# Optimization experiments

Hardware: AMD Instinct MI355X
Metric: run time of the kernel (lower is better)

## Reference

```python
import jax, jax.numpy as jnp
import numpy as np

B, T, D = 1, 2048, 1024
H = 16
SEM_DIM, GEO_DIM, ATTN_DIM = 512, 512, 1024
ROPE_BASE = 10000.0
NEG = -1e9


def setup_inputs() -> dict:
    key = jax.random.key(0)
    ks = jax.random.split(key, 10)
    s = 0.02
    return {
        "x": jax.random.normal(ks[0], (B, T, D), jnp.float32),
        "wq_sem": jax.random.normal(ks[1], (D, SEM_DIM), jnp.float32) * s,
        "wk_sem": jax.random.normal(ks[2], (D, SEM_DIM), jnp.float32) * s,
        "wq_geo": jax.random.normal(ks[3], (D, GEO_DIM), jnp.float32) * s,
        "wk_geo": jax.random.normal(ks[4], (D, GEO_DIM), jnp.float32) * s,
        "wv": jax.random.normal(ks[5], (D, ATTN_DIM), jnp.float32) * s,
        "wo": jax.random.normal(ks[6], (ATTN_DIM, D), jnp.float32) * s,
        "k_sem_null": jax.random.normal(ks[7], (SEM_DIM,), jnp.float32) * s,
        "k_geo_null": jax.random.normal(ks[8], (GEO_DIM,), jnp.float32) * s,
        "v_null": jax.random.normal(ks[9], (ATTN_DIM,), jnp.float32) * s,
    }


def _heads(y, hd):
    b, t, _ = y.shape
    return y.reshape(b, t, H, hd).transpose(0, 2, 1, 3)  # [B,H,T,hd]


def _rope(x, cos, sin):
    # x: [B,H,T,hd], cos/sin: [T,hd//2] (rotate-half convention)
    hd = x.shape[-1]
    x1, x2 = x[..., : hd // 2], x[..., hd // 2 :]
    c = cos[None, None]
    sn = sin[None, None]
    return jnp.concatenate([x1 * c - x2 * sn, x2 * c + x1 * sn], axis=-1)


def _forward(x, wq_sem, wk_sem, wq_geo, wk_geo, wv, wo, k_sem_null, k_geo_null, v_null):
    b, t, _ = x.shape
    sem_hd = wq_sem.shape[1] // H
    geo_hd = wq_geo.shape[1] // H
    v_hd = wv.shape[1] // H
    sem_scale = 1.0 / np.sqrt(sem_hd)
    geo_scale = 1.0 / np.sqrt(geo_hd)

    qs = _heads(x @ wq_sem, sem_hd)
    ks = _heads(x @ wk_sem, sem_hd)
    qg = _heads(x @ wq_geo, geo_hd)
    kg = _heads(x @ wk_geo, geo_hd)
    v = _heads(x @ wv, v_hd)

    # RoPE on geometric branch only
    pos = jnp.arange(t, dtype=jnp.float32)
    inv_freq = 1.0 / (ROPE_BASE ** (jnp.arange(0, geo_hd, 2, dtype=jnp.float32) / geo_hd))
    ang = pos[:, None] * inv_freq[None, :]  # [T, geo_hd//2]
    cos, sin = jnp.cos(ang), jnp.sin(ang)
    qg = _rope(qg, cos, sin)
    kg = _rope(kg, cos, sin)

    # prepend null KV slot (not rotated, always attendable)
    ksn = jnp.broadcast_to(k_sem_null.reshape(1, 1, H, sem_hd).transpose(0, 2, 1, 3), (b, H, 1, sem_hd))
    kgn = jnp.broadcast_to(k_geo_null.reshape(1, 1, H, geo_hd).transpose(0, 2, 1, 3), (b, H, 1, geo_hd))
    vn = jnp.broadcast_to(v_null.reshape(1, 1, H, v_hd).transpose(0, 2, 1, 3), (b, H, 1, v_hd))
    ks_full = jnp.concatenate([ksn, ks], axis=2)  # [B,H,T+1,sem_hd]
    kg_full = jnp.concatenate([kgn, kg], axis=2)
    v_full = jnp.concatenate([vn, v], axis=2)

    # decoupled scores in fp32: sem*sem_scale + geo*geo_scale
    scores = (
        jnp.einsum("bhqd,bhkd->bhqk", qs, ks_full).astype(jnp.float32) * sem_scale
        + jnp.einsum("bhqd,bhkd->bhqk", qg, kg_full).astype(jnp.float32) * geo_scale
    )

    # causal mask over real tokens; null slot (key index 0) always visible
    causal = jnp.tril(jnp.ones((t, t), dtype=bool))
    mask = jnp.concatenate([jnp.ones((t, 1), dtype=bool), causal], axis=1)  # [T, T+1]
    scores = jnp.where(mask[None, None], scores, NEG)

    probs = jax.nn.softmax(scores, axis=-1).astype(v.dtype)
    out = jnp.einsum("bhqk,bhkd->bhqd", probs, v_full)  # [B,H,T,v_hd]
    out = out.transpose(0, 2, 1, 3).reshape(b, t, H * v_hd)
    return out @ wo


def reference(x, wq_sem, wk_sem, wq_geo, wk_geo, wv, wo, k_sem_null, k_geo_null, v_null):
    return _forward(x, wq_sem, wk_sem, wq_geo, wk_geo, wv, wo, k_sem_null, k_geo_null, v_null)
```

## Files before the change

### kernel.cpp

```cpp
#include <hip/hip_runtime.h>
#include <hip/hip_bf16.h>

typedef __hip_bfloat16 bf16;
typedef __attribute__((ext_vector_type(8))) short bf16x8;
typedef __attribute__((ext_vector_type(4))) short bf16x4;
typedef __attribute__((ext_vector_type(4))) float f32x4;

#define TSEQ   2048
#define DMODEL 1024
#define NHEAD  16
#define KST    2112
#define SCALE  0.17677669529663687f
#define LN1E4_16 0.5756462732485115f

__device__ __forceinline__ unsigned short f2bf(float f) {
    union { bf16 h; unsigned short u; } x;
    x.h = __float2bfloat16(f);
    return x.u;
}
__device__ __forceinline__ float bf2f(unsigned short u) {
    return __uint_as_float(((unsigned int)u) << 16);
}

__device__ __forceinline__ void gload_lds16(const void* g, void* l) {
    __builtin_amdgcn_global_load_lds(
        (const __attribute__((address_space(1))) void*)g,
        (__attribute__((address_space(3))) void*)l, 16, 0, 0);
}

__global__ __launch_bounds__(256) void prep_all(
    const float* __restrict__ X,
    const float* __restrict__ wqs, const float* __restrict__ wks,
    const float* __restrict__ wqg, const float* __restrict__ wkg,
    const float* __restrict__ wv,  const float* __restrict__ wo,
    const float* __restrict__ ksn, const float* __restrict__ kgn,
    const float* __restrict__ vn,
    unsigned short* __restrict__ Xb,
    unsigned short* __restrict__ WcatT, unsigned short* __restrict__ WoT,
    unsigned short* __restrict__ Kc, unsigned short* __restrict__ Vg)
{
    __shared__ float T[64][65];
    const int bx = blockIdx.x;
    const int tid = threadIdx.x;
    if (bx < 2048) {
        int i = (bx * 256 + tid) * 4;
        float4 v = *(const float4*)(X + i);
        ushort4 o;
        o.x = f2bf(v.x); o.y = f2bf(v.y); o.z = f2bf(v.z); o.w = f2bf(v.w);
        *(ushort4*)(Xb + i) = o;
    } else if (bx < 3584) {
        const int idx = bx - 2048;
        const int z = idx >> 8, rem = idx & 255;
        const int cx = rem & 15, ry = rem >> 4;
        const float* src; unsigned short* dst; int C;
        switch (z) {
            case 0: src = wqs; dst = WcatT;               C = 512;  break;
            case 1: src = wks; dst = WcatT + 512  * 1024; C = 512;  break;
            case 2: src = wqg; dst = WcatT + 1024 * 1024; C = 512;  break;
            case 3: src = wkg; dst = WcatT + 1536 * 1024; C = 512;  break;
            case 4: src = wv;  dst = WcatT + 2048 * 1024; C = 1024; break;
            default: src = wo; dst = WoT;                 C = 1024; break;
        }
        const int c0 = cx * 64;
        if (c0 >= C) return;
        const int r0 = ry * 64;
        #pragma unroll
        for (int i = 0; i < 16; ++i) {
            int id2 = tid + 256 * i;
            int r = id2 >> 6, c = id2 & 63;
            T[r][c] = src[(size_t)(r0 + r) * C + c0 + c];
        }
        __syncthreads();
        #pragma unroll
        for (int i = 0; i < 16; ++i) {
            int id2 = tid + 256 * i;
            int cc = id2 >> 6, rr = id2 & 63;
            dst[(size_t)(c0 + cc) * 1024 + r0 + rr] = f2bf(T[rr][cc]);
        }
    } else {
        const int h = bx - 3584;
        const int d = tid & 63, g = tid >> 6;
        if (g == 0)
            Kc[((size_t)h * KST + 0) * 64 + d] =
                f2bf(d < 32 ? ksn[h * 32 + d] : kgn[h * 32 + d - 32]);
        if (g == 1)
            Vg[((size_t)h * 64 + d) * KST + 0] = f2bf(vn[h * 64 + d]);
        for (int fk = 2049 + g; fk < KST; fk += 4) {
            Kc[((size_t)h * KST + fk) * 64 + d] = 0;
            Vg[((size_t)h * 64 + d) * KST + fk] = 0;
        }
    }
}

__global__ __launch_bounds__(256) void gemm_proj_fused(
    const unsigned short* __restrict__ A,
    const unsigned short* __restrict__ Bt,
    unsigned short* __restrict__ Qc,
    unsigned short* __restrict__ Kc,
    unsigned short* __restrict__ Vg)
{
    __shared__ __align__(16) unsigned short Abuf[64 * 64];
    __shared__ __align__(16) unsigned short Bbuf[128 * 64];
    const int n0 = blockIdx.x * 128, m0 = blockIdx.y * 64;
    const int tid = threadIdx.x, l = tid & 63, wv = tid >> 6;
    const int wr = wv >> 1, wc = wv & 1;
    const int lr = l & 15, lg = l >> 4;

    f32x4 acc[2][4];
    #pragma unroll
    for (int i = 0; i < 2; ++i)
        #pragma unroll
        for (int j = 0; j < 4; ++j) acc[i][j] = (f32x4){0.f, 0.f, 0.f, 0.f};

    for (int k0 = 0; k0 < 1024; k0 += 64) {
        #pragma unroll
        for (int i = 0; i < 2; ++i) {
            int c = wv * 128 + i * 64 + l;
            int row = c >> 3, sseg = (c & 7) ^ (row & 7);
            gload_lds16(A + (size_t)(m0 + row) * 1024 + k0 + sseg * 8,
                        &Abuf[(wv * 128 + i * 64) * 8]);
        }
        #pragma unroll
        for (int i = 0; i < 4; ++i) {
            int c = wv * 256 + i * 64 + l;
            int row = c >> 3, sseg = (c & 7) ^ (row & 7);
            gload_lds16(Bt + (size_t)(n0 + row) * 1024 + k0 + sseg * 8,
                        &Bbuf[(wv * 256 + i * 64) * 8]);
        }
        __syncthreads();
        #pragma unroll
        for (int ks = 0; ks < 2; ++ks) {
            bf16x8 af[2], bfv[4];
            #pragma unroll
            for (int mf = 0; mf < 2; ++mf) {
                int rr = wr * 32 + mf * 16 + lr;
                int seg = (ks * 4 + lg) ^ (rr & 7);
                af[mf] = *(const bf16x8*)&Abuf[rr * 64 + seg * 8];
            }
            #pragma unroll
            for (int nf = 0; nf < 4; ++nf) {
                int rr = wc * 64 + nf * 16 + lr;
                int seg = (ks * 4 + lg) ^ (rr & 7);
                bfv[nf] = *(const bf16x8*)&Bbuf[rr * 64 + seg * 8];
            }
            #pragma unroll
            for (int mf = 0; mf < 2; ++mf)
                #pragma unroll
                for (int nf = 0; nf < 4; ++nf)
                    acc[mf][nf] = __builtin_amdgcn_mfma_f32_16x16x32_bf16(
                        af[mf], bfv[nf], acc[mf][nf], 0, 0, 0);
        }
        __syncthreads();
    }

    const int sec = n0 >> 9;
    if (sec <= 1) {
        unsigned short* dst = (sec == 0) ? Qc : Kc;
        const int tstr  = (sec == 0) ? TSEQ : KST;
        const int fkoff = (sec == 0) ? 0 : 1;
        const float sc  = (sec == 0) ? SCALE : 1.0f;
        #pragma unroll
        for (int mf = 0; mf < 2; ++mf)
            #pragma unroll
            for (int nf = 0; nf < 4; ++nf) {
                int col = (n0 & 511) + wc * 64 + nf * 16 + lr;
                int h = col >> 5, d = col & 31;
                #pragma unroll
                for (int reg = 0; reg < 4; ++reg) {
                    int q = m0 + wr * 32 + mf * 16 + lg * 4 + reg;
                    dst[((size_t)h * tstr + q + fkoff) * 64 + d] =
                        f2bf(acc[mf][nf][reg] * sc);
                }
            }
    } else if (sec <= 3) {
        unsigned short* dst = (sec == 2) ? Qc : Kc;
        const int tstr  = (sec == 2) ? TSEQ : KST;
        const int fkoff = (sec == 2) ? 0 : 1;
        const float sc  = (sec == 2) ? SCALE : 1.0f;
        const float invf = __expf(-(float)lr * LN1E4_16);
        #pragma unroll
        for (int mf = 0; mf < 2; ++mf)
            #pragma unroll
            for (int reg = 0; reg < 4; ++reg) {
                int q = m0 + wr * 32 + mf * 16 + lg * 4 + reg;
                float s, c;
                __sincosf((float)q * invf, &s, &c);
                #pragma unroll
                for (int nfp = 0; nfp < 2; ++nfp) {
                    int nf0 = nfp * 2;
                    int colbase = (n0 & 511) + wc * 64 + nf0 * 16;
                    int h = colbase >> 5;
                    float x1 = acc[mf][nf0][reg], x2 = acc[mf][nf0 + 1][reg];
                    size_t base = ((size_t)h * tstr + q + fkoff) * 64 + 32;
                    dst[base + lr]      = f2bf((x1 * c - x2 * s) * sc);
                    dst[base + lr + 16] = f2bf((x2 * c + x1 * s) * sc);
                }
            }
    } else {
        #pragma unroll
        for (int nf = 0; nf < 4; ++nf) {
            int colr = (n0 - 2048) + wc * 64 + nf * 16 + lr;
            int h = colr >> 6, dv = colr & 63;
            size_t rowbase = ((size_t)h * 64 + dv) * KST;
            #pragma unroll
            for (int mf = 0; mf < 2; ++mf)
                #pragma unroll
                for (int reg = 0; reg < 4; ++reg) {
                    int q = m0 + wr * 32 + mf * 16 + lg * 4 + reg;
                    Vg[rowbase + q + 1] = f2bf(acc[mf][nf][reg]);
                }
        }
    }
}

__global__ __launch_bounds__(256) void gemm_out(const unsigned short* __restrict__ A,
                                                const unsigned short* __restrict__ Bt,
                                                float* __restrict__ C)
{
    __shared__ __align__(16) unsigned short Abuf[64 * 64];
    __shared__ __align__(16) unsigned short Bbuf[128 * 64];
    const int n0 = blockIdx.x * 128, m0 = blockIdx.y * 64;
    const int tid = threadIdx.x, l = tid & 63, wv = tid >> 6;
    const int wr = wv >> 1, wc = wv & 1;
    const int lr = l & 15, lg = l >> 4;

    f32x4 acc[2][4];
    #pragma unroll
    for (int i = 0; i < 2; ++i)
        #pragma unroll
        for (int j = 0; j < 4; ++j) acc[i][j] = (f32x4){0.f, 0.f, 0.f, 0.f};

    for (int k0 = 0; k0 < 1024; k0 += 64) {
        #pragma unroll
        for (int i = 0; i < 2; ++i) {
            int c = wv * 128 + i * 64 + l;
            int row = c >> 3, sseg = (c & 7) ^ (row & 7);
            gload_lds16(A + (size_t)(m0 + row) * 1024 + k0 + sseg * 8,
                        &Abuf[(wv * 128 + i * 64) * 8]);
        }
        #pragma unroll
        for (int i = 0; i < 4; ++i) {
            int c = wv * 256 + i * 64 + l;
            int row = c >> 3, sseg = (c & 7) ^ (row & 7);
            gload_lds16(Bt + (size_t)(n0 + row) * 1024 + k0 + sseg * 8,
                        &Bbuf[(wv * 256 + i * 64) * 8]);
        }
        __syncthreads();
        #pragma unroll
        for (int ks = 0; ks < 2; ++ks) {
            bf16x8 af[2], bfv[4];
            #pragma unroll
            for (int mf = 0; mf < 2; ++mf) {
                int rr = wr * 32 + mf * 16 + lr;
                int seg = (ks * 4 + lg) ^ (rr & 7);
                af[mf] = *(const bf16x8*)&Abuf[rr * 64 + seg * 8];
            }
            #pragma unroll
            for (int nf = 0; nf < 4; ++nf) {
                int rr = wc * 64 + nf * 16 + lr;
                int seg = (ks * 4 + lg) ^ (rr & 7);
                bfv[nf] = *(const bf16x8*)&Bbuf[rr * 64 + seg * 8];
            }
            #pragma unroll
            for (int mf = 0; mf < 2; ++mf)
                #pragma unroll
                for (int nf = 0; nf < 4; ++nf)
                    acc[mf][nf] = __builtin_amdgcn_mfma_f32_16x16x32_bf16(
                        af[mf], bfv[nf], acc[mf][nf], 0, 0, 0);
        }
        __syncthreads();
    }
    #pragma unroll
    for (int mf = 0; mf < 2; ++mf)
        #pragma unroll
        for (int nf = 0; nf < 4; ++nf)
            #pragma unroll
            for (int reg = 0; reg < 4; ++reg) {
                int row = m0 + wr * 32 + mf * 16 + lg * 4 + reg;
                int col = n0 + wc * 64 + nf * 16 + lr;
                C[(size_t)row * DMODEL + col] = acc[mf][nf][reg];
            }
}

__global__ __launch_bounds__(256) void attn_mfma(
    const unsigned short* __restrict__ Qc,
    const unsigned short* __restrict__ Kc,
    const unsigned short* __restrict__ Vg,
    unsigned short* __restrict__ attnO,
    unsigned short* __restrict__ OpA,
    unsigned short* __restrict__ OpB,
    float2* __restrict__ ml)
{
    __shared__ __align__(16) unsigned short KsL[2][64 * 64];
    __shared__ __align__(16) unsigned short VsL[2][64 * 64];
    __shared__ __align__(16) unsigned short Ps[128 * 64];

    const int ib = blockIdx.x;
    const int hp = ib & 7;
    const int j  = ib >> 3;
    const int h  = hp * 2 + (j & 1);
    const int item = j >> 1;

    int qb, part, np;
    {
        int i = item;
        if (i < 16)      { np = 4; qb = 15 - (i >> 2); part = i & 3; }
        else if (i < 28) { int jj = i - 16; np = 3; qb = 11 - jj / 3; part = jj % 3; }
        else if (i < 38) { int jj = i - 28; np = 2; qb = 7 - (jj >> 1); part = jj & 1; }
        else             { np = 1; qb = 2 - (i - 38); part = 0; }
    }
    const int nt = 2 * qb + 3;
    const int bsz = nt / np, rem = nt % np;
    const int t0 = part * bsz + (part < rem ? part : rem);
    const int t1 = t0 + bsz + (part < rem ? 1 : 0);

    const int q0 = qb * 128;
    const int tid = threadIdx.x, l = tid & 63, w = tid >> 6;
    const int lr = l & 15, lg = l >> 4;

    bf16x8 qa[2][2];
    #pragma unroll
    for (int rg = 0; rg < 2; ++rg) {
        int qr = q0 + w * 32 + rg * 16 + lr;
        qa[rg][0] = *(const bf16x8*)&Qc[((size_t)h * TSEQ + qr) * 64 + lg * 8];
        qa[rg][1] = *(const bf16x8*)&Qc[((size_t)h * TSEQ + qr) * 64 + 32 + lg * 8];
    }

    const int sc8 = (((l & 7) ^ ((l >> 3) & 7))) * 8;
    const int r0s = (w * 2 + 0) * 8 + (l >> 3);
    const int r1s = (w * 2 + 1) * 8 + (l >> 3);
    const unsigned short* Kh = Kc + (((size_t)h * KST) << 6);
    const unsigned short* Vh = Vg + (size_t)h * 64 * KST;

#define STAGE_KV(bufi, fk0_) do {                                              \
        gload_lds16(Kh + (((size_t)((fk0_) + r0s)) << 6) + sc8,                \
                    &KsL[bufi][(w * 2 + 0) * 512]);                            \
        gload_lds16(Kh + (((size_t)((fk0_) + r1s)) << 6) + sc8,                \
                    &KsL[bufi][(w * 2 + 1) * 512]);                            \
        gload_lds16(Vh + (size_t)r0s * KST + (fk0_) + sc8,                     \
                    &VsL[bufi][(w * 2 + 0) * 512]);                            \
        gload_lds16(Vh + (size_t)r1s * KST + (fk0_) + sc8,                     \
                    &VsL[bufi][(w * 2 + 1) * 512]);                            \
    } while (0)

    f32x4 o[2][4];
    #pragma unroll
    for (int rg = 0; rg < 2; ++rg)
        #pragma unroll
        for (int i = 0; i < 4; ++i) o[rg][i] = (f32x4){0.f, 0.f, 0.f, 0.f};
    float m[2]  = {-1e30f, -1e30f};
    float ll[2] = {0.f, 0.f};

    int buf = 0;
    STAGE_KV(0, t0 * 64);
    asm volatile("s_waitcnt vmcnt(0)" ::: "memory");
    __builtin_amdgcn_s_barrier();

    for (int kb = t0; kb < t1; ++kb) {
        const int fk0 = kb * 64;
        if (kb + 1 < t1) STAGE_KV(buf ^ 1, fk0 + 64);

        const unsigned short* Ksb = &KsL[buf][0];
        const unsigned short* Vsb = &VsL[buf][0];

        f32x4 sa[2][4];
        #pragma unroll
        for (int rg = 0; rg < 2; ++rg)
            #pragma unroll
            for (int i = 0; i < 4; ++i) sa[rg][i] = (f32x4){0.f, 0.f, 0.f, 0.f};
        __builtin_amdgcn_s_setprio(1);
        #pragma unroll
        for (int ks = 0; ks < 2; ++ks) {
            int dd = lg * 8 + ks * 32;
            #pragma unroll
            for (int nf = 0; nf < 4; ++nf) {
                int kkc = nf * 16 + lr;
                bf16x8 kbf = *(const bf16x8*)&Ksb[kkc * 64 + (dd ^ ((kkc & 7) << 3))];
                sa[0][nf] = __builtin_amdgcn_mfma_f32_16x16x32_bf16(kbf, qa[0][ks], sa[0][nf], 0, 0, 0);
                sa[1][nf] = __builtin_amdgcn_mfma_f32_16x16x32_bf16(kbf, qa[1][ks], sa[1][nf], 0, 0, 0);
            }
        }
        __builtin_amdgcn_s_setprio(0);

        const bool needmask = (fk0 + 62 > q0 + w * 32);
        #pragma unroll
        for (int rg = 0; rg < 2; ++rg) {
            const int q = q0 + w * 32 + rg * 16 + lr;
            float mt = -1e30f;
            if (needmask) {
                #pragma unroll
                for (int nf = 0; nf < 4; ++nf)
                    #pragma unroll
                    for (int reg = 0; reg < 4; ++reg) {
                        int fk = fk0 + nf * 16 + lg * 4 + reg;
                        float val = (fk <= q + 1) ? sa[rg][nf][reg] : -1e9f;
                        sa[rg][nf][reg] = val;
                        mt = fmaxf(mt, val);
                    }
            } else {
                #pragma unroll
                for (int nf = 0; nf < 4; ++nf)
                    #pragma unroll
                    for (int reg = 0; reg < 4; ++reg)
                        mt = fmaxf(mt, sa[rg][nf][reg]);
            }
            mt = fmaxf(mt, __shfl_xor(mt, 16, 64));
            mt = fmaxf(mt, __shfl_xor(mt, 32, 64));
            if (__any(mt > m[rg] + 8.0f)) {
                float mn = fmaxf(m[rg], mt);
                float alpha = __expf(m[rg] - mn);
                m[rg] = mn;
                ll[rg] *= alpha;
                #pragma unroll
                for (int nf = 0; nf < 4; ++nf)
                    #pragma unroll
                    for (int reg = 0; reg < 4; ++reg)
                        o[rg][nf][reg] *= alpha;
            }
            float rs = 0.0f;
            #pragma unroll
            for (int nf = 0; nf < 4; ++nf)
                #pragma unroll
                for (int reg = 0; reg < 4; ++reg) {
                    float p = __expf(sa[rg][nf][reg] - m[rg]);
                    sa[rg][nf][reg] = p;
                    rs += p;
                }
            rs += __shfl_xor(rs, 16, 64);
            rs += __shfl_xor(rs, 32, 64);
            ll[rg] += rs;

            int r = w * 32 + rg * 16 + lr;
            #pragma unroll
            for (int nf = 0; nf < 4; ++nf) {
                bf16x4 pk;
                pk[0] = f2bf(sa[rg][nf][0]); pk[1] = f2bf(sa[rg][nf][1]);
                pk[2] = f2bf(sa[rg][nf][2]); pk[3] = f2bf(sa[rg][nf][3]);
                int kk0 = nf * 16 + lg * 4;
                *(bf16x4*)&Ps[r * 64 + (kk0 ^ ((r & 7) << 3))] = pk;
            }
        }

        __builtin_amdgcn_s_setprio(1);
        #pragma unroll
        for (int ks = 0; ks < 2; ++ks) {
            int kk0 = lg * 8 + ks * 32;
            int swz = kk0 ^ ((lr & 7) << 3);
            bf16x8 pa0 = *(const bf16x8*)&Ps[(w * 32 + lr) * 64 + swz];
            bf16x8 pa1 = *(const bf16x8*)&Ps[(w * 32 + 16 + lr) * 64 + swz];
            #pragma unroll
            for (int nf = 0; nf < 4; ++nf) {
                int dv = nf * 16 + lr;
                bf16x8 vb = *(const bf16x8*)&Vsb[dv * 64 + (kk0 ^ ((dv & 7) << 3))];
                o[0][nf] = __builtin_amdgcn_mfma_f32_16x16x32_bf16(vb, pa0, o[0][nf], 0, 0, 0);
                o[1][nf] = __builtin_amdgcn_mfma_f32_16x16x32_bf16(vb, pa1, o[1][nf], 0, 0, 0);
            }
        }
        __builtin_amdgcn_s_setprio(0);

        asm volatile("s_waitcnt vmcnt(0)" ::: "memory");
        __builtin_amdgcn_s_barrier();
        buf ^= 1;
    }
#undef STAGE_KV

    const int sidx = h * 38 + item;
    unsigned short* Od = (np == 1) ? 0
        : ((sidx < 384) ? OpA + (size_t)sidx * 8192
                        : OpB + (size_t)(sidx - 384) * 8192);
    #pragma unroll
    for (int rg = 0; rg < 2; ++rg) {
        const float inv = 1.0f / ll[rg];
        const int q = q0 + w * 32 + rg * 16 + lr;
        if (np == 1) {
            #pragma unroll
            for (int nf = 0; nf < 4; ++nf) {
                ushort4 ov;
                ov.x = f2bf(o[rg][nf][0] * inv); ov.y = f2bf(o[rg][nf][1] * inv);
                ov.z = f2bf(o[rg][nf][2] * inv); ov.w = f2bf(o[rg][nf][3] * inv);
                *(ushort4*)&attnO[(size_t)q * DMODEL + h * 64 + nf * 16 + lg * 4] = ov;
            }
        } else {
            const int r = w * 32 + rg * 16 + lr;
            #pragma unroll
            for (int nf = 0; nf < 4; ++nf) {
                ushort4 ov;
                ov.x = f2bf(o[rg][nf][0] * inv); ov.y = f2bf(o[rg][nf][1] * inv);
                ov.z = f2bf(o[rg][nf][2] * inv); ov.w = f2bf(o[rg][nf][3] * inv);
                *(ushort4*)&Od[r * 64 + nf * 16 + lg * 4] = ov;
            }
            if (lg == 0)
                ml[sidx * 128 + r] = make_float2(m[rg], ll[rg]);
        }
    }
}

__global__ __launch_bounds__(256) void combine_wave(
    const unsigned short* __restrict__ OpA,
    const unsigned short* __restrict__ OpB,
    const float2* __restrict__ ml,
    unsigned short* __restrict__ attnO)
{
    const int qb = 3 + blockIdx.x;
    const int h  = blockIdx.y;
    int np, i0;
    if (qb >= 12)     { np = 4; i0 = (15 - qb) * 4; }
    else if (qb >= 8) { np = 3; i0 = 16 + (11 - qb) * 3; }
    else              { np = 2; i0 = 28 + (7 - qb) * 2; }
    const int sidx0 = h * 38 + i0;

    const int t = threadIdx.x;
    const int r = t & 127, dv0 = (t >> 7) * 32;

    float wt[4];
    float mm = -1e30f;
    #pragma unroll
    for (int p = 0; p < 4; ++p)
        if (p < np) mm = fmaxf(mm, ml[(sidx0 + p) * 128 + r].x);
    float tot = 0.0f;
    #pragma unroll
    for (int p = 0; p < 4; ++p) {
        wt[p] = 0.0f;
        if (p < np) {
            float2 v = ml[(sidx0 + p) * 128 + r];
            wt[p] = v.y * __expf(v.x - mm);
            tot += wt[p];
        }
    }
    const float inv = 1.0f / tot;

    float accv[32];
    #pragma unroll
    for (int c = 0; c < 32; ++c) accv[c] = 0.0f;
    #pragma unroll
    for (int p = 0; p < 4; ++p) {
        if (p < np) {
            int s = sidx0 + p;
            const unsigned short* Od = (s < 384)
                ? OpA + (size_t)s * 8192
                : OpB + (size_t)(s - 384) * 8192;
            #pragma unroll
            for (int c4 = 0; c4 < 8; ++c4) {
                ushort4 v = *(const ushort4*)&Od[r * 64 + dv0 + c4 * 4];
                accv[c4 * 4 + 0] += wt[p] * bf2f(v.x);
                accv[c4 * 4 + 1] += wt[p] * bf2f(v.y);
                accv[c4 * 4 + 2] += wt[p] * bf2f(v.z);
                accv[c4 * 4 + 3] += wt[p] * bf2f(v.w);
            }
        }
    }
    const int q = qb * 128 + r;
    #pragma unroll
    for (int c4 = 0; c4 < 8; ++c4) {
        ushort4 ov;
        ov.x = f2bf(accv[c4 * 4 + 0] * inv);
        ov.y = f2bf(accv[c4 * 4 + 1] * inv);
        ov.z = f2bf(accv[c4 * 4 + 2] * inv);
        ov.w = f2bf(accv[c4 * 4 + 3] * inv);
        *(ushort4*)&attnO[(size_t)q * DMODEL + h * 64 + dv0 + c4 * 4] = ov;
    }
}

extern "C" void kernel_launch(void* const* d_in, const int* in_sizes, int n_in,
                              void* d_out, int out_size, void* d_ws, size_t ws_size,
                              hipStream_t stream)
{
    const float* x      = (const float*)d_in[0];
    const float* wq_sem = (const float*)d_in[1];
    const float* wk_sem = (const float*)d_in[2];
    const float* wq_geo = (const float*)d_in[3];
    const float* wk_geo = (const float*)d_in[4];
    const float* wv     = (const float*)d_in[5];
    const float* wo     = (const float*)d_in[6];
    const float* ksn    = (const float*)d_in[7];
    const float* kgn    = (const float*)d_in[8];
    const float* vn     = (const float*)d_in[9];
    float* out = (float*)d_out;

    char* ws = (char*)d_ws;
    unsigned short* Xb    = (unsigned short*)(ws);
    unsigned short* attnO = (unsigned short*)(ws);
    unsigned short* WcatT = (unsigned short*)(ws + 4194304);
    unsigned short* OpA   = (unsigned short*)(ws + 4194304);
    unsigned short* WoT   = (unsigned short*)(ws + 10485760);
    unsigned short* Qc    = (unsigned short*)(ws + 12582912);
    unsigned short* Kc    = (unsigned short*)(ws + 16777216);
    unsigned short* Vg    = (unsigned short*)(ws + 21102592);
    unsigned short* OpB   = (unsigned short*)(ws + 25427968);
    float2*         ml    = (float2*)(ws + 29097984);

    prep_all<<<3600, 256, 0, stream>>>(x, wq_sem, wk_sem, wq_geo, wk_geo, wv, wo,
                                       ksn, kgn, vn, Xb, WcatT, WoT, Kc, Vg);

    gemm_proj_fused<<<dim3(24, 32), 256, 0, stream>>>(Xb, WcatT, Qc, Kc, Vg);

    attn_mfma<<<656, 256, 0, stream>>>(Qc, Kc, Vg, attnO, OpA, OpB, ml);
    combine_wave<<<dim3(13, NHEAD), 256, 0, stream>>>(OpA, OpB, ml, attnO);

    gemm_out<<<dim3(8, 32), 256, 0, stream>>>(attnO, WoT, out);
}
```

Measured before the change: 91.09 us.

## Prefetch K two tiles ahead, hoist V reads, shrink P buffer per row group

The attention kernel now triple-buffers K and double-buffers V, issuing K loads two tiles ahead with a partial vmcnt wait so the next K tile is ready before V finishes. V fragments are read from LDS into registers at the start of each iteration. The P staging buffer is halved by writing and immediately consuming probabilities one row group at a time. Launch bounds now request 3 blocks per CU, and the s_setprio hints are removed. These changes aim to hide global-load latency and raise occupancy, at the cost of higher register pressure and an intra-wave LDS write-then-read dependency on P.

```diff
diff --git a/kernel.cpp b/kernel.cpp
--- a/kernel.cpp
+++ b/kernel.cpp
@@ -282,7 +282,7 @@
             }
 }
 
-__global__ __launch_bounds__(256) void attn_mfma(
+__global__ __launch_bounds__(256, 3) void attn_mfma(
     const unsigned short* __restrict__ Qc,
     const unsigned short* __restrict__ Kc,
     const unsigned short* __restrict__ Vg,
@@ -291,9 +291,9 @@
     unsigned short* __restrict__ OpB,
     float2* __restrict__ ml)
 {
-    __shared__ __align__(16) unsigned short KsL[2][64 * 64];
+    __shared__ __align__(16) unsigned short KsL[3][64 * 64];
     __shared__ __align__(16) unsigned short VsL[2][64 * 64];
-    __shared__ __align__(16) unsigned short Ps[128 * 64];
+    __shared__ __align__(16) unsigned short Ps[64 * 64];
 
     const int ib = blockIdx.x;
     const int hp = ib & 7;
@@ -332,11 +332,13 @@
     const unsigned short* Kh = Kc + (((size_t)h * KST) << 6);
     const unsigned short* Vh = Vg + (size_t)h * 64 * KST;
 
-#define STAGE_KV(bufi, fk0_) do {                                              \
+#define STAGE_K(bufi, fk0_) do {                                               \
         gload_lds16(Kh + (((size_t)((fk0_) + r0s)) << 6) + sc8,                \
                     &KsL[bufi][(w * 2 + 0) * 512]);                            \
         gload_lds16(Kh + (((size_t)((fk0_) + r1s)) << 6) + sc8,                \
                     &KsL[bufi][(w * 2 + 1) * 512]);                            \
+    } while (0)
+#define STAGE_V(bufi, fk0_) do {                                               \
         gload_lds16(Vh + (size_t)r0s * KST + (fk0_) + sc8,                     \
                     &VsL[bufi][(w * 2 + 0) * 512]);                            \
         gload_lds16(Vh + (size_t)r1s * KST + (fk0_) + sc8,                     \
@@ -351,24 +353,36 @@
     float m[2]  = {-1e30f, -1e30f};
     float ll[2] = {0.f, 0.f};
 
-    int buf = 0;
-    STAGE_KV(0, t0 * 64);
-    asm volatile("s_waitcnt vmcnt(0)" ::: "memory");
+    STAGE_K(t0 % 3, t0 * 64);
+    STAGE_V(t0 & 1, t0 * 64);
+    STAGE_K((t0 + 1) % 3, (t0 + 1) * 64);
+    asm volatile("s_waitcnt vmcnt(2)" ::: "memory");
     __builtin_amdgcn_s_barrier();
 
     for (int kb = t0; kb < t1; ++kb) {
         const int fk0 = kb * 64;
-        if (kb + 1 < t1) STAGE_KV(buf ^ 1, fk0 + 64);
-
-        const unsigned short* Ksb = &KsL[buf][0];
-        const unsigned short* Vsb = &VsL[buf][0];
+        const unsigned short* Ksb = &KsL[kb % 3][0];
+        const unsigned short* Vsb = &VsL[kb & 1][0];
+        const bool moreV = (kb + 1 < t1);
+        const bool moreK = (kb + 2 < t1);
+        if (moreV) STAGE_V((kb + 1) & 1, fk0 + 64);
+        if (moreK) STAGE_K((kb + 2) % 3, fk0 + 128);
+
+        bf16x8 vb[2][4];
+        #pragma unroll
+        for (int ks = 0; ks < 2; ++ks)
+            #pragma unroll
+            for (int nf = 0; nf < 4; ++nf) {
+                int dv = nf * 16 + lr;
+                vb[ks][nf] = *(const bf16x8*)
+                    &Vsb[dv * 64 + ((lg * 8 + ks * 32) ^ ((dv & 7) << 3))];
+            }
 
         f32x4 sa[2][4];
         #pragma unroll
         for (int rg = 0; rg < 2; ++rg)
             #pragma unroll
             for (int i = 0; i < 4; ++i) sa[rg][i] = (f32x4){0.f, 0.f, 0.f, 0.f};
-        __builtin_amdgcn_s_setprio(1);
         #pragma unroll
         for (int ks = 0; ks < 2; ++ks) {
             int dd = lg * 8 + ks * 32;
@@ -380,9 +394,10 @@
                 sa[1][nf] = __builtin_amdgcn_mfma_f32_16x16x32_bf16(kbf, qa[1][ks], sa[1][nf], 0, 0, 0);
             }
         }
-        __builtin_amdgcn_s_setprio(0);
 
         const bool needmask = (fk0 + 62 > q0 + w * 32);
+        const int pr = w * 16 + lr;
+        const int psw = (pr & 7) << 3;
         #pragma unroll
         for (int rg = 0; rg < 2; ++rg) {
             const int q = q0 + w * 32 + rg * 16 + lr;
@@ -430,39 +445,31 @@
             rs += __shfl_xor(rs, 32, 64);
             ll[rg] += rs;
 
-            int r = w * 32 + rg * 16 + lr;
             #pragma unroll
             for (int nf = 0; nf < 4; ++nf) {
                 bf16x4 pk;
                 pk[0] = f2bf(sa[rg][nf][0]); pk[1] = f2bf(sa[rg][nf][1]);
                 pk[2] = f2bf(sa[rg][nf][2]); pk[3] = f2bf(sa[rg][nf][3]);
                 int kk0 = nf * 16 + lg * 4;
-                *(bf16x4*)&Ps[r * 64 + (kk0 ^ ((r & 7) << 3))] = pk;
-            }
-        }
-
-        __builtin_amdgcn_s_setprio(1);
-        #pragma unroll
-        for (int ks = 0; ks < 2; ++ks) {
-            int kk0 = lg * 8 + ks * 32;
-            int swz = kk0 ^ ((lr & 7) << 3);
-            bf16x8 pa0 = *(const bf16x8*)&Ps[(w * 32 + lr) * 64 + swz];
-            bf16x8 pa1 = *(const bf16x8*)&Ps[(w * 32 + 16 + lr) * 64 + swz];
-            #pragma unroll
-            for (int nf = 0; nf < 4; ++nf) {
-                int dv = nf * 16 + lr;
-                bf16x8 vb = *(const bf16x8*)&Vsb[dv * 64 + (kk0 ^ ((dv & 7) << 3))];
-                o[0][nf] = __builtin_amdgcn_mfma_f32_16x16x32_bf16(vb, pa0, o[0][nf], 0, 0, 0);
-                o[1][nf] = __builtin_amdgcn_mfma_f32_16x16x32_bf16(vb, pa1, o[1][nf], 0, 0, 0);
-            }
-        }
-        __builtin_amdgcn_s_setprio(0);
-
-        asm volatile("s_waitcnt vmcnt(0)" ::: "memory");
+                *(bf16x4*)&Ps[pr * 64 + (kk0 ^ psw)] = pk;
+            }
+            #pragma unroll
+            for (int ks = 0; ks < 2; ++ks) {
+                int kk0 = lg * 8 + ks * 32;
+                bf16x8 pa = *(const bf16x8*)&Ps[pr * 64 + (kk0 ^ psw)];
+                #pragma unroll
+                for (int nf = 0; nf < 4; ++nf)
+                    o[rg][nf] = __builtin_amdgcn_mfma_f32_16x16x32_bf16(
+                        vb[ks][nf], pa, o[rg][nf], 0, 0, 0);
+            }
+        }
+
+        if (moreK) { asm volatile("s_waitcnt vmcnt(2)" ::: "memory"); }
+        else       { asm volatile("s_waitcnt vmcnt(0)" ::: "memory"); }
         __builtin_amdgcn_s_barrier();
-        buf ^= 1;
-    }
-#undef STAGE_KV
+    }
+#undef STAGE_K
+#undef STAGE_V
 
     const int sidx = h * 38 + item;
     unsigned short* Od = (np == 1) ? 0
```

After: 84.16 us, median of 2. -7.6%, faster.
